# Performance work log

Measured on AMD Instinct MI355X. Metric: run time of the kernel, lower is better.

## Reference

```python
import jax, jax.numpy as jnp
import numpy as np

B, D_MODEL, N, H = 2, 1024, 2048, 16
HEAD_DIM = D_MODEL // H  # 64


def _proj(x, W, b):
    # Conv1d kernel_size=1 == per-position GEMM over channels. x: [B, Cin, N]
    return jnp.einsum('oi,bin->bon', W, x) + b[:, None]


def setup_inputs() -> dict:
    key = jax.random.key(0)
    ks = jax.random.split(key, 11)
    s = 1.0 / np.sqrt(D_MODEL)
    mk = lambda k: (jax.random.uniform(k, (D_MODEL, D_MODEL), jnp.float32, -s, s))
    return {
        'query': jax.random.normal(ks[0], (B, D_MODEL, N), jnp.float32),
        'key': jax.random.normal(ks[1], (B, D_MODEL, N), jnp.float32),
        'value': jax.random.normal(ks[2], (B, D_MODEL, N), jnp.float32),
        'Wq': mk(ks[3]), 'bq': jax.random.uniform(ks[4], (D_MODEL,), jnp.float32, -s, s),
        'Wk': mk(ks[5]), 'bk': jax.random.uniform(ks[6], (D_MODEL,), jnp.float32, -s, s),
        'Wv': mk(ks[7]), 'bv': jax.random.uniform(ks[8], (D_MODEL,), jnp.float32, -s, s),
        'Wm': mk(ks[9]), 'bm': jax.random.uniform(ks[10], (D_MODEL,), jnp.float32, -s, s),
    }


def reference(query, key, value, Wq, bq, Wk, bk, Wv, bv, Wm, bm):
    b = query.shape[0]
    # project then split channels as (head_dim, heads) exactly like torch .view
    q = _proj(query, Wq, bq).reshape(b, HEAD_DIM, H, -1)  # [B, d, H, N]
    k = _proj(key, Wk, bk).reshape(b, HEAD_DIM, H, -1)
    v = _proj(value, Wv, bv).reshape(b, HEAD_DIM, H, -1)
    scores = jnp.einsum('bdhn,bdhm->bhnm', q, k) / np.sqrt(HEAD_DIM).astype(np.float32)
    prob = jax.nn.softmax(scores, axis=-1)  # [B, H, N, N]
    x = jnp.einsum('bhnm,bdhm->bdhn', prob, v)  # [B, d, H, N]
    return _proj(x.reshape(b, D_MODEL, -1), Wm, bm)  # [B, d_model, N]
```

## Files before the change

kernel.cpp:

```cpp
#include <hip/hip_runtime.h>
#include <stdint.h>

#define DM 1024
#define NS 2048
#define NH 16
#define HD 64
#define SQ 72

typedef unsigned short u16;
typedef __attribute__((ext_vector_type(8))) short short8;
typedef __attribute__((ext_vector_type(8))) unsigned short u16x8;
typedef __attribute__((ext_vector_type(4))) float f32x4;
typedef __attribute__((ext_vector_type(4))) unsigned short u16x4;

static __device__ __forceinline__ u16 f2bf(float f) {
  union { float f; uint32_t i; } x; x.f = f;
  return (u16)((x.i + 0x7fffu + ((x.i >> 16) & 1u)) >> 16);
}
static __device__ __forceinline__ void gload16(u16* lds, const u16* g) {
  auto l = (__attribute__((address_space(3))) uint32_t*)(uint32_t)(uintptr_t)lds;
  auto gp = (const __attribute__((address_space(1))) uint32_t*)(uintptr_t)g;
  __builtin_amdgcn_global_load_lds(gp, l, 16, 0, 0);
}

__global__ __launch_bounds__(256) void cvt4_k(const float* __restrict__ a,
                                              const float* __restrict__ b,
                                              const float* __restrict__ c,
                                              const float* __restrict__ d,
                                              u16* __restrict__ oa, u16* __restrict__ ob,
                                              u16* __restrict__ oc, u16* __restrict__ od) {
  const int y = blockIdx.y;
  const float* in = y == 0 ? a : y == 1 ? b : y == 2 ? c : d;
  u16* out = y == 0 ? oa : y == 1 ? ob : y == 2 ? oc : od;
  int i = (blockIdx.x * 256 + threadIdx.x) * 4;
  f32x4 v = *(const f32x4*)(in + i);
  u16x4 o;
  o.x = f2bf(v.x); o.y = f2bf(v.y); o.z = f2bf(v.z); o.w = f2bf(v.w);
  *(u16x4*)(out + i) = o;
}

__global__ __launch_bounds__(256) void trf3_k(const float* __restrict__ q,
                                              const float* __restrict__ k,
                                              const float* __restrict__ v,
                                              u16* __restrict__ oq, u16* __restrict__ ok,
                                              u16* __restrict__ ov) {
  __shared__ __attribute__((aligned(16))) u16 t[64][65];
  const int z = blockIdx.z, b = z & 1, which = z >> 1;
  const float* in = which == 0 ? q : which == 1 ? k : v;
  u16* out = which == 0 ? oq : which == 1 ? ok : ov;
  const float* ip = in + (size_t)b * DM * NS;
  u16* op = out + (size_t)b * DM * NS;
  const int r0 = blockIdx.y * 64, c0 = blockIdx.x * 64;
  const int tx = threadIdx.x, ty = threadIdx.y;
#pragma unroll
  for (int j = 0; j < 4; ++j) {
    int row = ty + j * 16;
    f32x4 vv = *(const f32x4*)(ip + (size_t)(r0 + row) * NS + c0 + tx * 4);
    t[row][tx * 4 + 0] = f2bf(vv.x); t[row][tx * 4 + 1] = f2bf(vv.y);
    t[row][tx * 4 + 2] = f2bf(vv.z); t[row][tx * 4 + 3] = f2bf(vv.w);
  }
  __syncthreads();
#pragma unroll
  for (int j = 0; j < 4; ++j) {
    int crow = ty + j * 16;
    u16x4 vv;
    vv.x = t[tx * 4 + 0][crow]; vv.y = t[tx * 4 + 1][crow];
    vv.z = t[tx * 4 + 2][crow]; vv.w = t[tx * 4 + 3][crow];
    *(u16x4*)(op + (size_t)(c0 + crow) * DM + r0 + tx * 4) = vv;
  }
}

__global__ __launch_bounds__(256) void tr_k(const u16* __restrict__ in,
                                            u16* __restrict__ out) {
  __shared__ __attribute__((aligned(16))) u16 t[64][65];
  const int b = blockIdx.z;
  const u16* ip = in + (size_t)b * DM * NS;
  u16* op = out + (size_t)b * DM * NS;
  const int r0 = blockIdx.y * 64, c0 = blockIdx.x * 64;
  const int tx = threadIdx.x, ty = threadIdx.y;
#pragma unroll
  for (int j = 0; j < 4; ++j) {
    int row = ty + j * 16;
    u16x4 v = *(const u16x4*)(ip + (size_t)(r0 + row) * NS + c0 + tx * 4);
    t[row][tx * 4 + 0] = v.x; t[row][tx * 4 + 1] = v.y;
    t[row][tx * 4 + 2] = v.z; t[row][tx * 4 + 3] = v.w;
  }
  __syncthreads();
#pragma unroll
  for (int j = 0; j < 4; ++j) {
    int crow = ty + j * 16;
    u16x4 v;
    v.x = t[tx * 4 + 0][crow]; v.y = t[tx * 4 + 1][crow];
    v.z = t[tx * 4 + 2][crow]; v.w = t[tx * 4 + 3][crow];
    *(u16x4*)(op + (size_t)(c0 + crow) * DM + r0 + tx * 4) = v;
  }
}

__global__ __launch_bounds__(256) void qkv_k(
    const u16* __restrict__ Xq, const u16* __restrict__ Xk, const u16* __restrict__ Xv,
    const u16* __restrict__ Wq, const u16* __restrict__ Wk, const u16* __restrict__ Wv,
    const float* __restrict__ bq, const float* __restrict__ bk, const float* __restrict__ bv,
    u16* __restrict__ QH, u16* __restrict__ KH, u16* __restrict__ VH) {
  __shared__ __attribute__((aligned(16))) u16 As[128 * 32];
  __shared__ __attribute__((aligned(16))) u16 Bs[128 * 32];
  const int z = blockIdx.z, b = z & 1, which = z >> 1;
  const u16* X = which == 0 ? Xq : which == 1 ? Xk : Xv;
  const u16* W = which == 0 ? Wq : which == 1 ? Wk : Wv;
  const float* bias = which == 0 ? bq : which == 1 ? bk : bv;
  u16* out = which == 0 ? QH : which == 1 ? KH : VH;
  const int m0 = blockIdx.x * 128;
  const int c0 = blockIdx.y * 128;
  const u16* Xb = X + (size_t)b * NS * DM;
  const int tid = threadIdx.x;
  const int lane = tid & 63, w = tid >> 6;
  const int wm = w >> 1, wc = w & 1;
  const int qd = lane >> 4, ml = lane & 15;

  f32x4 acc[4][4];
#pragma unroll
  for (int i = 0; i < 4; ++i)
#pragma unroll
    for (int j = 0; j < 4; ++j) acc[i][j] = (f32x4){0.f, 0.f, 0.f, 0.f};

  for (int k0 = 0; k0 < DM; k0 += 32) {
    __syncthreads();
#pragma unroll
    for (int it = 0; it < 2; ++it) {
      int ci = it * 256 + tid;
      int row = ci >> 2, j = ci & 3;
      gload16(&As[ci * 8], Xb + (size_t)(m0 + row) * DM + k0 + j * 8);
      gload16(&Bs[ci * 8], W + (size_t)(c0 + row) * DM + k0 + j * 8);
    }
    __syncthreads();
    short8 af[4], bf[4];
#pragma unroll
    for (int i = 0; i < 4; ++i) {
      af[i] = *(const short8*)&As[(wm * 64 + i * 16 + ml) * 32 + qd * 8];
      bf[i] = *(const short8*)&Bs[(wc * 64 + i * 16 + ml) * 32 + qd * 8];
    }
#pragma unroll
    for (int mi = 0; mi < 4; ++mi)
#pragma unroll
      for (int ci2 = 0; ci2 < 4; ++ci2)
        acc[mi][ci2] = __builtin_amdgcn_mfma_f32_16x16x32_bf16(af[mi], bf[ci2],
                                                               acc[mi][ci2], 0, 0, 0);
  }

  const int cw = c0 + wc * 64;
  const int mw = m0 + wm * 64;
  float bv4[4];
#pragma unroll
  for (int ci2 = 0; ci2 < 4; ++ci2) bv4[ci2] = bias[cw + ci2 * 16 + ml];

  if (which < 2) {
    const int h = ml, d0 = cw >> 4;
    u16* ob = out + ((size_t)(b * NH + h) * NS) * HD;
#pragma unroll
    for (int mi = 0; mi < 4; ++mi) {
#pragma unroll
      for (int r = 0; r < 4; ++r) {
        int n = mw + mi * 16 + qd * 4 + r;
        u16x4 v;
        v.x = f2bf(acc[mi][0][r] + bv4[0]); v.y = f2bf(acc[mi][1][r] + bv4[1]);
        v.z = f2bf(acc[mi][2][r] + bv4[2]); v.w = f2bf(acc[mi][3][r] + bv4[3]);
        *(u16x4*)(ob + (size_t)n * HD + d0) = v;
      }
    }
  } else {
#pragma unroll
    for (int ci2 = 0; ci2 < 4; ++ci2) {
      int c = cw + ci2 * 16 + ml;
      int h = c & 15, d = c >> 4;
#pragma unroll
      for (int mi = 0; mi < 4; ++mi) {
        int nb = mw + mi * 16 + qd * 4;
        u16x4 v;
        v.x = f2bf(acc[mi][ci2][0] + bv4[ci2]); v.y = f2bf(acc[mi][ci2][1] + bv4[ci2]);
        v.z = f2bf(acc[mi][ci2][2] + bv4[ci2]); v.w = f2bf(acc[mi][ci2][3] + bv4[ci2]);
        *(u16x4*)(out + ((size_t)(b * NH + h) * HD + d) * NS + nb) = v;
      }
    }
  }
}

__global__ __launch_bounds__(256) void proj_o(const u16* __restrict__ X,
                                              const u16* __restrict__ W,
                                              const float* __restrict__ bias,
                                              float* __restrict__ out) {
  __shared__ __attribute__((aligned(16))) u16 As[128 * 32];
  __shared__ __attribute__((aligned(16))) u16 Bs[128 * 32];
  const int b = blockIdx.z;
  const int m0 = blockIdx.x * 128;
  const int c0 = blockIdx.y * 128;
  const u16* Xb = X + (size_t)b * NS * DM;
  const int tid = threadIdx.x;
  const int lane = tid & 63, w = tid >> 6;
  const int wm = w >> 1, wc = w & 1;
  const int qd = lane >> 4, ml = lane & 15;

  f32x4 acc[4][4];
#pragma unroll
  for (int i = 0; i < 4; ++i)
#pragma unroll
    for (int j = 0; j < 4; ++j) acc[i][j] = (f32x4){0.f, 0.f, 0.f, 0.f};

  for (int k0 = 0; k0 < DM; k0 += 32) {
    __syncthreads();
#pragma unroll
    for (int it = 0; it < 2; ++it) {
      int ci = it * 256 + tid;
      int row = ci >> 2, j = ci & 3;
      gload16(&As[ci * 8], Xb + (size_t)(m0 + row) * DM + k0 + j * 8);
      gload16(&Bs[ci * 8], W + (size_t)(c0 + row) * DM + k0 + j * 8);
    }
    __syncthreads();
    short8 af[4], bf[4];
#pragma unroll
    for (int i = 0; i < 4; ++i) {
      af[i] = *(const short8*)&As[(wm * 64 + i * 16 + ml) * 32 + qd * 8];
      bf[i] = *(const short8*)&Bs[(wc * 64 + i * 16 + ml) * 32 + qd * 8];
    }
#pragma unroll
    for (int mi = 0; mi < 4; ++mi)
#pragma unroll
      for (int ci2 = 0; ci2 < 4; ++ci2)
        acc[mi][ci2] = __builtin_amdgcn_mfma_f32_16x16x32_bf16(af[mi], bf[ci2],
                                                               acc[mi][ci2], 0, 0, 0);
  }

  const int cw = c0 + wc * 64;
  const int mw = m0 + wm * 64;
#pragma unroll
  for (int ci2 = 0; ci2 < 4; ++ci2) {
    int c = cw + ci2 * 16 + ml;
    float bv = bias[c];
#pragma unroll
    for (int mi = 0; mi < 4; ++mi) {
      int nb = mw + mi * 16 + qd * 4;
      f32x4 v;
      v.x = acc[mi][ci2][0] + bv; v.y = acc[mi][ci2][1] + bv;
      v.z = acc[mi][ci2][2] + bv; v.w = acc[mi][ci2][3] + bv;
      *(f32x4*)(out + ((size_t)b * DM + c) * NS + nb) = v;
    }
  }
}

__global__ __launch_bounds__(256) void attn_k(const u16* __restrict__ Q,
                                              const u16* __restrict__ K,
                                              const u16* __restrict__ V,
                                              u16* __restrict__ XO) {
  __shared__ __attribute__((aligned(16))) u16 QPs[64 * SQ];
  __shared__ __attribute__((aligned(16))) u16 Ks[64 * SQ];
  __shared__ __attribute__((aligned(16))) u16 Vs[64 * SQ];
  const int bh = blockIdx.y, b = bh >> 4, h = bh & 15;
  const int n0 = blockIdx.x * 64;
  const u16* Qb = Q + (size_t)bh * NS * HD;
  const u16* Kb = K + (size_t)bh * NS * HD;
  const u16* Vb = V + (size_t)bh * HD * NS;
  const int tid = threadIdx.x, lane = tid & 63, w = tid >> 6;
  const int qd = lane >> 4, ml = lane & 15;

#pragma unroll
  for (int it = 0; it < 2; ++it) {
    int ci = it * 256 + tid;
    int row = ci >> 3, j = ci & 7;
    *(u16x8*)&QPs[row * SQ + j * 8] = *(const u16x8*)(Qb + (size_t)(n0 + row) * HD + j * 8);
  }
  __syncthreads();
  short8 aq[2];
#pragma unroll
  for (int ks = 0; ks < 2; ++ks)
    aq[ks] = *(const short8*)&QPs[(w * 16 + ml) * SQ + (ks * 4 + qd) * 8];

  f32x4 O[4];
#pragma unroll
  for (int i = 0; i < 4; ++i) O[i] = (f32x4){0.f, 0.f, 0.f, 0.f};
  float lsum[4] = {0.f, 0.f, 0.f, 0.f};
  const float SC = 0.125f * 1.44269504088896340736f;

  const int srow = tid >> 3, sj = tid & 7;

  for (int kb = 0; kb < NS / 64; ++kb) {
    u16x8 kv[2], vv[2];
#pragma unroll
    for (int it = 0; it < 2; ++it) {
      kv[it] = *(const u16x8*)(Kb + (size_t)(kb * 64 + srow + it * 32) * HD + sj * 8);
      vv[it] = *(const u16x8*)(Vb + (size_t)(srow + it * 32) * NS + kb * 64 + sj * 8);
    }
    __syncthreads();
#pragma unroll
    for (int it = 0; it < 2; ++it) {
      *(u16x8*)&Ks[(srow + it * 32) * SQ + sj * 8] = kv[it];
      *(u16x8*)&Vs[(srow + it * 32) * SQ + sj * 8] = vv[it];
    }
    __syncthreads();

    f32x4 S[4];
#pragma unroll
    for (int f = 0; f < 4; ++f) S[f] = (f32x4){0.f, 0.f, 0.f, 0.f};
#pragma unroll
    for (int f = 0; f < 4; ++f)
#pragma unroll
      for (int ks = 0; ks < 2; ++ks) {
        short8 bk = *(const short8*)&Ks[(f * 16 + ml) * SQ + (ks * 4 + qd) * 8];
        S[f] = __builtin_amdgcn_mfma_f32_16x16x32_bf16(aq[ks], bk, S[f], 0, 0, 0);
      }

#pragma unroll
    for (int f = 0; f < 4; ++f)
#pragma unroll
      for (int r = 0; r < 4; ++r) {
        float p = __builtin_amdgcn_exp2f(S[f][r] * SC);
        QPs[(w * 16 + qd * 4 + r) * SQ + f * 16 + ml] = f2bf(p);
        lsum[r] += p;
      }
    __syncthreads();

#pragma unroll
    for (int kk = 0; kk < 2; ++kk) {
      short8 ap = *(const short8*)&QPs[(w * 16 + ml) * SQ + (kk * 4 + qd) * 8];
#pragma unroll
      for (int df = 0; df < 4; ++df) {
        short8 bvv = *(const short8*)&Vs[(df * 16 + ml) * SQ + (kk * 4 + qd) * 8];
        O[df] = __builtin_amdgcn_mfma_f32_16x16x32_bf16(ap, bvv, O[df], 0, 0, 0);
      }
    }
  }

#pragma unroll
  for (int off = 1; off < 16; off <<= 1)
#pragma unroll
    for (int r = 0; r < 4; ++r) lsum[r] += __shfl_xor(lsum[r], off);
#pragma unroll
  for (int r = 0; r < 4; ++r) lsum[r] = 1.f / lsum[r];

  const int nb = n0 + w * 16 + qd * 4;
#pragma unroll
  for (int df = 0; df < 4; ++df) {
    int d = df * 16 + ml;
    int c = d * NH + h;
    u16x4 v;
    v.x = f2bf(O[df][0] * lsum[0]); v.y = f2bf(O[df][1] * lsum[1]);
    v.z = f2bf(O[df][2] * lsum[2]); v.w = f2bf(O[df][3] * lsum[3]);
    *(u16x4*)(XO + ((size_t)b * DM + c) * NS + nb) = v;
  }
}

extern "C" void kernel_launch(void* const* d_in, const int* in_sizes, int n_in,
                              void* d_out, int out_size, void* d_ws, size_t ws_size,
                              hipStream_t stream) {
  const float* query = (const float*)d_in[0];
  const float* key = (const float*)d_in[1];
  const float* value = (const float*)d_in[2];
  const float* Wq = (const float*)d_in[3]; const float* bq = (const float*)d_in[4];
  const float* Wk = (const float*)d_in[5]; const float* bk = (const float*)d_in[6];
  const float* Wv = (const float*)d_in[7]; const float* bv = (const float*)d_in[8];
  const float* Wm = (const float*)d_in[9]; const float* bm = (const float*)d_in[10];

  u16* ws = (u16*)d_ws;
  const size_t TS = (size_t)2 * NS * DM;
  const size_t WSZ = (size_t)DM * DM;
  u16* XTq = ws;
  u16* XTk = ws + TS;
  u16* XTv = ws + 2 * TS;
  u16* QH = ws + 3 * TS;
  u16* KH = ws + 4 * TS;
  u16* VH = ws + 5 * TS;
  u16* Wqb = ws + 6 * TS;
  u16* Wkb = Wqb + WSZ;
  u16* Wvb = Wkb + WSZ;
  u16* Wmb = Wvb + WSZ;
  u16* XO = XTq;
  u16* XOT = XTk;

  cvt4_k<<<dim3(WSZ / 1024, 4), 256, 0, stream>>>(Wq, Wk, Wv, Wm, Wqb, Wkb, Wvb, Wmb);

  dim3 tb(16, 16);
  trf3_k<<<dim3(NS / 64, DM / 64, 6), tb, 0, stream>>>(query, key, value, XTq, XTk, XTv);

  qkv_k<<<dim3(NS / 128, DM / 128, 6), 256, 0, stream>>>(
      XTq, XTk, XTv, Wqb, Wkb, Wvb, bq, bk, bv, QH, KH, VH);

  attn_k<<<dim3(NS / 64, 32), 256, 0, stream>>>(QH, KH, VH, XO);

  tr_k<<<dim3(NS / 64, DM / 64, 2), tb, 0, stream>>>(XO, XOT);
  proj_o<<<dim3(NS / 128, DM / 128, 2), 256, 0, stream>>>(XOT, Wmb, bm, (float*)d_out);
}
```

Baseline: 262.9 us.

## Split attention over key halves with combine kernel, fold softmax scale into Q

```diff
diff --git a/kernel.cpp b/kernel.cpp
--- a/kernel.cpp
+++ b/kernel.cpp
@@ -108,6 +108,7 @@
   const u16* W = which == 0 ? Wq : which == 1 ? Wk : Wv;
   const float* bias = which == 0 ? bq : which == 1 ? bk : bv;
   u16* out = which == 0 ? QH : which == 1 ? KH : VH;
+  const float sc = which == 0 ? 0.18033688011112042f : 1.0f;
   const int m0 = blockIdx.x * 128;
   const int c0 = blockIdx.y * 128;
   const u16* Xb = X + (size_t)b * NS * DM;
@@ -161,8 +162,10 @@
       for (int r = 0; r < 4; ++r) {
         int n = mw + mi * 16 + qd * 4 + r;
         u16x4 v;
-        v.x = f2bf(acc[mi][0][r] + bv4[0]); v.y = f2bf(acc[mi][1][r] + bv4[1]);
-        v.z = f2bf(acc[mi][2][r] + bv4[2]); v.w = f2bf(acc[mi][3][r] + bv4[3]);
+        v.x = f2bf((acc[mi][0][r] + bv4[0]) * sc);
+        v.y = f2bf((acc[mi][1][r] + bv4[1]) * sc);
+        v.z = f2bf((acc[mi][2][r] + bv4[2]) * sc);
+        v.w = f2bf((acc[mi][3][r] + bv4[3]) * sc);
         *(u16x4*)(ob + (size_t)n * HD + d0) = v;
       }
     }
@@ -187,10 +190,10 @@
                                               const u16* __restrict__ W,
                                               const float* __restrict__ bias,
                                               float* __restrict__ out) {
-  __shared__ __attribute__((aligned(16))) u16 As[128 * 32];
+  __shared__ __attribute__((aligned(16))) u16 As[64 * 32];
   __shared__ __attribute__((aligned(16))) u16 Bs[128 * 32];
   const int b = blockIdx.z;
-  const int m0 = blockIdx.x * 128;
+  const int m0 = blockIdx.x * 64;
   const int c0 = blockIdx.y * 128;
   const u16* Xb = X + (size_t)b * NS * DM;
   const int tid = threadIdx.x;
@@ -198,30 +201,34 @@
   const int wm = w >> 1, wc = w & 1;
   const int qd = lane >> 4, ml = lane & 15;
 
-  f32x4 acc[4][4];
-#pragma unroll
-  for (int i = 0; i < 4; ++i)
+  f32x4 acc[2][4];
+#pragma unroll
+  for (int i = 0; i < 2; ++i)
 #pragma unroll
     for (int j = 0; j < 4; ++j) acc[i][j] = (f32x4){0.f, 0.f, 0.f, 0.f};
 
   for (int k0 = 0; k0 < DM; k0 += 32) {
     __syncthreads();
+    {
+      int row = tid >> 2, j = tid & 3;
+      gload16(&As[tid * 8], Xb + (size_t)(m0 + row) * DM + k0 + j * 8);
+    }
 #pragma unroll
     for (int it = 0; it < 2; ++it) {
       int ci = it * 256 + tid;
       int row = ci >> 2, j = ci & 3;
-      gload16(&As[ci * 8], Xb + (size_t)(m0 + row) * DM + k0 + j * 8);
       gload16(&Bs[ci * 8], W + (size_t)(c0 + row) * DM + k0 + j * 8);
     }
     __syncthreads();
-    short8 af[4], bf[4];
-#pragma unroll
-    for (int i = 0; i < 4; ++i) {
-      af[i] = *(const short8*)&As[(wm * 64 + i * 16 + ml) * 32 + qd * 8];
+    short8 af[2], bf[4];
+#pragma unroll
+    for (int i = 0; i < 2; ++i)
+      af[i] = *(const short8*)&As[(wm * 32 + i * 16 + ml) * 32 + qd * 8];
+#pragma unroll
+    for (int i = 0; i < 4; ++i)
       bf[i] = *(const short8*)&Bs[(wc * 64 + i * 16 + ml) * 32 + qd * 8];
-    }
-#pragma unroll
-    for (int mi = 0; mi < 4; ++mi)
+#pragma unroll
+    for (int mi = 0; mi < 2; ++mi)
 #pragma unroll
       for (int ci2 = 0; ci2 < 4; ++ci2)
         acc[mi][ci2] = __builtin_amdgcn_mfma_f32_16x16x32_bf16(af[mi], bf[ci2],
@@ -229,13 +236,13 @@
   }
 
   const int cw = c0 + wc * 64;
-  const int mw = m0 + wm * 64;
+  const int mw = m0 + wm * 32;
 #pragma unroll
   for (int ci2 = 0; ci2 < 4; ++ci2) {
     int c = cw + ci2 * 16 + ml;
     float bv = bias[c];
 #pragma unroll
-    for (int mi = 0; mi < 4; ++mi) {
+    for (int mi = 0; mi < 2; ++mi) {
       int nb = mw + mi * 16 + qd * 4;
       f32x4 v;
       v.x = acc[mi][ci2][0] + bv; v.y = acc[mi][ci2][1] + bv;
@@ -248,15 +255,18 @@
 __global__ __launch_bounds__(256) void attn_k(const u16* __restrict__ Q,
                                               const u16* __restrict__ K,
                                               const u16* __restrict__ V,
-                                              u16* __restrict__ XO) {
+                                              float* __restrict__ O0,
+                                              float* __restrict__ O1,
+                                              float* __restrict__ lp) {
   __shared__ __attribute__((aligned(16))) u16 QPs[64 * SQ];
   __shared__ __attribute__((aligned(16))) u16 Ks[64 * SQ];
   __shared__ __attribute__((aligned(16))) u16 Vs[64 * SQ];
   const int bh = blockIdx.y, b = bh >> 4, h = bh & 15;
+  const int half = blockIdx.z;
   const int n0 = blockIdx.x * 64;
   const u16* Qb = Q + (size_t)bh * NS * HD;
-  const u16* Kb = K + (size_t)bh * NS * HD;
-  const u16* Vb = V + (size_t)bh * HD * NS;
+  const u16* Kb = K + (size_t)bh * NS * HD + (size_t)half * (NS / 2) * HD;
+  const u16* Vb = V + (size_t)bh * HD * NS + (size_t)half * (NS / 2);
   const int tid = threadIdx.x, lane = tid & 63, w = tid >> 6;
   const int qd = lane >> 4, ml = lane & 15;
 
@@ -276,11 +286,10 @@
 #pragma unroll
   for (int i = 0; i < 4; ++i) O[i] = (f32x4){0.f, 0.f, 0.f, 0.f};
   float lsum[4] = {0.f, 0.f, 0.f, 0.f};
-  const float SC = 0.125f * 1.44269504088896340736f;
 
   const int srow = tid >> 3, sj = tid & 7;
 
-  for (int kb = 0; kb < NS / 64; ++kb) {
+  for (int kb = 0; kb < (NS / 2) / 64; ++kb) {
     u16x8 kv[2], vv[2];
 #pragma unroll
     for (int it = 0; it < 2; ++it) {
@@ -310,7 +319,7 @@
     for (int f = 0; f < 4; ++f)
 #pragma unroll
       for (int r = 0; r < 4; ++r) {
-        float p = __builtin_amdgcn_exp2f(S[f][r] * SC);
+        float p = __builtin_amdgcn_exp2f(S[f][r]);
         QPs[(w * 16 + qd * 4 + r) * SQ + f * 16 + ml] = f2bf(p);
         lsum[r] += p;
       }
@@ -331,19 +340,40 @@
   for (int off = 1; off < 16; off <<= 1)
 #pragma unroll
     for (int r = 0; r < 4; ++r) lsum[r] += __shfl_xor(lsum[r], off);
-#pragma unroll
-  for (int r = 0; r < 4; ++r) lsum[r] = 1.f / lsum[r];
-
+
+  float* Op = half ? O1 : O0;
   const int nb = n0 + w * 16 + qd * 4;
+  if (ml == 0) {
+    f32x4 lv = {lsum[0], lsum[1], lsum[2], lsum[3]};
+    *(f32x4*)(lp + ((size_t)(half * 32 + bh)) * NS + nb) = lv;
+  }
 #pragma unroll
   for (int df = 0; df < 4; ++df) {
     int d = df * 16 + ml;
     int c = d * NH + h;
-    u16x4 v;
-    v.x = f2bf(O[df][0] * lsum[0]); v.y = f2bf(O[df][1] * lsum[1]);
-    v.z = f2bf(O[df][2] * lsum[2]); v.w = f2bf(O[df][3] * lsum[3]);
-    *(u16x4*)(XO + ((size_t)b * DM + c) * NS + nb) = v;
-  }
+    *(f32x4*)(Op + ((size_t)b * DM + c) * NS + nb) = O[df];
+  }
+}
+
+__global__ __launch_bounds__(256) void comb_k(const float* __restrict__ O0,
+                                              const float* __restrict__ O1,
+                                              const float* __restrict__ lp,
+                                              u16* __restrict__ XO) {
+  const size_t t = (size_t)blockIdx.x * 256 + threadIdx.x;
+  const int n4 = (int)(t & (NS / 4 - 1));
+  const int c = (int)((t >> 9) & (DM - 1));
+  const int b = (int)(t >> 19);
+  const int h = c & 15;
+  f32x4 o0 = *(const f32x4*)(O0 + t * 4);
+  f32x4 o1 = *(const f32x4*)(O1 + t * 4);
+  f32x4 l0 = *(const f32x4*)(lp + ((size_t)(b * 16 + h)) * NS + n4 * 4);
+  f32x4 l1 = *(const f32x4*)(lp + ((size_t)(32 + b * 16 + h)) * NS + n4 * 4);
+  u16x4 v;
+  v.x = f2bf((o0.x + o1.x) / (l0.x + l1.x));
+  v.y = f2bf((o0.y + o1.y) / (l0.y + l1.y));
+  v.z = f2bf((o0.z + o1.z) / (l0.z + l1.z));
+  v.w = f2bf((o0.w + o1.w) / (l0.w + l1.w));
+  *(u16x4*)(XO + t * 4) = v;
 }
 
 extern "C" void kernel_launch(void* const* d_in, const int* in_sizes, int n_in,
@@ -370,8 +400,11 @@
   u16* Wkb = Wqb + WSZ;
   u16* Wvb = Wkb + WSZ;
   u16* Wmb = Wvb + WSZ;
-  u16* XO = XTq;
-  u16* XOT = XTk;
+  float* O0 = (float*)ws;
+  float* O1 = (float*)(ws + 6 * TS + 4 * WSZ);
+  float* lp = O1 + (size_t)2 * DM * NS;
+  u16* XO = XTv;
+  u16* XOT = QH;
 
   cvt4_k<<<dim3(WSZ / 1024, 4), 256, 0, stream>>>(Wq, Wk, Wv, Wm, Wqb, Wkb, Wvb, Wmb);
 
@@ -381,8 +414,10 @@
   qkv_k<<<dim3(NS / 128, DM / 128, 6), 256, 0, stream>>>(
       XTq, XTk, XTv, Wqb, Wkb, Wvb, bq, bk, bv, QH, KH, VH);
 
-  attn_k<<<dim3(NS / 64, 32), 256, 0, stream>>>(QH, KH, VH, XO);
+  attn_k<<<dim3(NS / 64, 32, 2), 256, 0, stream>>>(QH, KH, VH, O0, O1, lp);
+
+  comb_k<<<dim3((DM * NS * 2 / 4) / 256), 256, 0, stream>>>(O0, O1, lp, XO);
 
   tr_k<<<dim3(NS / 64, DM / 64, 2), tb, 0, stream>>>(XO, XOT);
-  proj_o<<<dim3(NS / 128, DM / 128, 2), 256, 0, stream>>>(XOT, Wmb, bm, (float*)d_out);
-}
+  proj_o<<<dim3(NS / 64, DM / 128, 2), 256, 0, stream>>>(XOT, Wmb, bm, (float*)d_out);
+}
```

Result: no change. 266.8 us (+1.5%).

## Restructure attention with double-buffered async K/V loads and register-resident P

Applied to the files above, without the earlier changes.

```diff
diff --git a/kernel.cpp b/kernel.cpp
--- a/kernel.cpp
+++ b/kernel.cpp
@@ -5,13 +5,15 @@
 #define NS 2048
 #define NH 16
 #define HD 64
-#define SQ 72
 
 typedef unsigned short u16;
 typedef __attribute__((ext_vector_type(8))) short short8;
+typedef __attribute__((ext_vector_type(4))) short s16x4;
 typedef __attribute__((ext_vector_type(8))) unsigned short u16x8;
 typedef __attribute__((ext_vector_type(4))) float f32x4;
 typedef __attribute__((ext_vector_type(4))) unsigned short u16x4;
+
+#define MFMA_PV(a, b, c) __builtin_amdgcn_mfma_f32_16x16x16bf16_1k(a, b, c, 0, 0, 0)
 
 static __device__ __forceinline__ u16 f2bf(float f) {
   union { float f; uint32_t i; } x; x.f = f;
@@ -108,6 +110,7 @@
   const u16* W = which == 0 ? Wq : which == 1 ? Wk : Wv;
   const float* bias = which == 0 ? bq : which == 1 ? bk : bv;
   u16* out = which == 0 ? QH : which == 1 ? KH : VH;
+  const float sc = which == 0 ? 0.18033688011112042f : 1.0f;
   const int m0 = blockIdx.x * 128;
   const int c0 = blockIdx.y * 128;
   const u16* Xb = X + (size_t)b * NS * DM;
@@ -161,8 +164,10 @@
       for (int r = 0; r < 4; ++r) {
         int n = mw + mi * 16 + qd * 4 + r;
         u16x4 v;
-        v.x = f2bf(acc[mi][0][r] + bv4[0]); v.y = f2bf(acc[mi][1][r] + bv4[1]);
-        v.z = f2bf(acc[mi][2][r] + bv4[2]); v.w = f2bf(acc[mi][3][r] + bv4[3]);
+        v.x = f2bf((acc[mi][0][r] + bv4[0]) * sc);
+        v.y = f2bf((acc[mi][1][r] + bv4[1]) * sc);
+        v.z = f2bf((acc[mi][2][r] + bv4[2]) * sc);
+        v.w = f2bf((acc[mi][3][r] + bv4[3]) * sc);
         *(u16x4*)(ob + (size_t)n * HD + d0) = v;
       }
     }
@@ -187,10 +192,10 @@
                                               const u16* __restrict__ W,
                                               const float* __restrict__ bias,
                                               float* __restrict__ out) {
-  __shared__ __attribute__((aligned(16))) u16 As[128 * 32];
+  __shared__ __attribute__((aligned(16))) u16 As[64 * 32];
   __shared__ __attribute__((aligned(16))) u16 Bs[128 * 32];
   const int b = blockIdx.z;
-  const int m0 = blockIdx.x * 128;
+  const int m0 = blockIdx.x * 64;
   const int c0 = blockIdx.y * 128;
   const u16* Xb = X + (size_t)b * NS * DM;
   const int tid = threadIdx.x;
@@ -198,30 +203,34 @@
   const int wm = w >> 1, wc = w & 1;
   const int qd = lane >> 4, ml = lane & 15;
 
-  f32x4 acc[4][4];
-#pragma unroll
-  for (int i = 0; i < 4; ++i)
+  f32x4 acc[2][4];
+#pragma unroll
+  for (int i = 0; i < 2; ++i)
 #pragma unroll
     for (int j = 0; j < 4; ++j) acc[i][j] = (f32x4){0.f, 0.f, 0.f, 0.f};
 
   for (int k0 = 0; k0 < DM; k0 += 32) {
     __syncthreads();
+    {
+      int row = tid >> 2, j = tid & 3;
+      gload16(&As[tid * 8], Xb + (size_t)(m0 + row) * DM + k0 + j * 8);
+    }
 #pragma unroll
     for (int it = 0; it < 2; ++it) {
       int ci = it * 256 + tid;
       int row = ci >> 2, j = ci & 3;
-      gload16(&As[ci * 8], Xb + (size_t)(m0 + row) * DM + k0 + j * 8);
       gload16(&Bs[ci * 8], W + (size_t)(c0 + row) * DM + k0 + j * 8);
     }
     __syncthreads();
-    short8 af[4], bf[4];
-#pragma unroll
-    for (int i = 0; i < 4; ++i) {
-      af[i] = *(const short8*)&As[(wm * 64 + i * 16 + ml) * 32 + qd * 8];
+    short8 af[2], bf[4];
+#pragma unroll
+    for (int i = 0; i < 2; ++i)
+      af[i] = *(const short8*)&As[(wm * 32 + i * 16 + ml) * 32 + qd * 8];
+#pragma unroll
+    for (int i = 0; i < 4; ++i)
       bf[i] = *(const short8*)&Bs[(wc * 64 + i * 16 + ml) * 32 + qd * 8];
-    }
-#pragma unroll
-    for (int mi = 0; mi < 4; ++mi)
+#pragma unroll
+    for (int mi = 0; mi < 2; ++mi)
 #pragma unroll
       for (int ci2 = 0; ci2 < 4; ++ci2)
         acc[mi][ci2] = __builtin_amdgcn_mfma_f32_16x16x32_bf16(af[mi], bf[ci2],
@@ -229,13 +238,13 @@
   }
 
   const int cw = c0 + wc * 64;
-  const int mw = m0 + wm * 64;
+  const int mw = m0 + wm * 32;
 #pragma unroll
   for (int ci2 = 0; ci2 < 4; ++ci2) {
     int c = cw + ci2 * 16 + ml;
     float bv = bias[c];
 #pragma unroll
-    for (int mi = 0; mi < 4; ++mi) {
+    for (int mi = 0; mi < 2; ++mi) {
       int nb = mw + mi * 16 + qd * 4;
       f32x4 v;
       v.x = acc[mi][ci2][0] + bv; v.y = acc[mi][ci2][1] + bv;
@@ -249,9 +258,8 @@
                                               const u16* __restrict__ K,
                                               const u16* __restrict__ V,
                                               u16* __restrict__ XO) {
-  __shared__ __attribute__((aligned(16))) u16 QPs[64 * SQ];
-  __shared__ __attribute__((aligned(16))) u16 Ks[64 * SQ];
-  __shared__ __attribute__((aligned(16))) u16 Vs[64 * SQ];
+  __shared__ __attribute__((aligned(16))) u16 Ks[2 * 2 * 2048];
+  __shared__ __attribute__((aligned(16))) u16 Vs[2 * 2 * 2048];
   const int bh = blockIdx.y, b = bh >> 4, h = bh & 15;
   const int n0 = blockIdx.x * 64;
   const u16* Qb = Q + (size_t)bh * NS * HD;
@@ -260,79 +268,86 @@
   const int tid = threadIdx.x, lane = tid & 63, w = tid >> 6;
   const int qd = lane >> 4, ml = lane & 15;
 
-#pragma unroll
-  for (int it = 0; it < 2; ++it) {
-    int ci = it * 256 + tid;
-    int row = ci >> 3, j = ci & 7;
-    *(u16x8*)&QPs[row * SQ + j * 8] = *(const u16x8*)(Qb + (size_t)(n0 + row) * HD + j * 8);
+  short8 aq[2];
+  {
+    const u16* qr = Qb + (size_t)(n0 + w * 16 + ml) * HD + qd * 8;
+    aq[0] = *(const short8*)qr;
+    aq[1] = *(const short8*)(qr + 32);
+  }
+
+  const int srow = tid >> 2, sjj = tid & 3;
+  const int vjj = sjj ^ (srow & 3);
+
+#pragma unroll
+  for (int s = 0; s < 2; ++s) {
+    gload16(&Ks[s * 2048 + tid * 8], Kb + (size_t)srow * HD + s * 32 + sjj * 8);
+    gload16(&Vs[s * 2048 + tid * 8], Vb + (size_t)srow * NS + s * 32 + vjj * 8);
   }
   __syncthreads();
-  short8 aq[2];
-#pragma unroll
-  for (int ks = 0; ks < 2; ++ks)
-    aq[ks] = *(const short8*)&QPs[(w * 16 + ml) * SQ + (ks * 4 + qd) * 8];
 
   f32x4 O[4];
 #pragma unroll
   for (int i = 0; i < 4; ++i) O[i] = (f32x4){0.f, 0.f, 0.f, 0.f};
-  float lsum[4] = {0.f, 0.f, 0.f, 0.f};
-  const float SC = 0.125f * 1.44269504088896340736f;
-
-  const int srow = tid >> 3, sj = tid & 7;
+  float lsum = 0.f;
+
+  const int vperm[2] = {(qd >> 1) ^ (ml & 3), (2 + (qd >> 1)) ^ (ml & 3)};
+  const int vhalf = (qd & 1) * 4;
 
   for (int kb = 0; kb < NS / 64; ++kb) {
-    u16x8 kv[2], vv[2];
-#pragma unroll
-    for (int it = 0; it < 2; ++it) {
-      kv[it] = *(const u16x8*)(Kb + (size_t)(kb * 64 + srow + it * 32) * HD + sj * 8);
-      vv[it] = *(const u16x8*)(Vb + (size_t)(srow + it * 32) * NS + kb * 64 + sj * 8);
+    const int cur = kb & 1, nxt = cur ^ 1;
+    if (kb < NS / 64 - 1) {
+#pragma unroll
+      for (int s = 0; s < 2; ++s) {
+        gload16(&Ks[(nxt * 2 + s) * 2048 + tid * 8],
+                Kb + (size_t)((kb + 1) * 64 + srow) * HD + s * 32 + sjj * 8);
+        gload16(&Vs[(nxt * 2 + s) * 2048 + tid * 8],
+                Vb + (size_t)srow * NS + (kb + 1) * 64 + s * 32 + vjj * 8);
+      }
+    }
+
+    const u16* kbase = &Ks[cur * 2 * 2048];
+    f32x4 S[4];
+#pragma unroll
+    for (int f = 0; f < 4; ++f) S[f] = (f32x4){0.f, 0.f, 0.f, 0.f};
+#pragma unroll
+    for (int f = 0; f < 4; ++f)
+#pragma unroll
+      for (int ks = 0; ks < 2; ++ks) {
+        short8 bk = *(const short8*)&kbase[ks * 2048 + (f * 16 + ml) * 32 + qd * 8];
+        S[f] = __builtin_amdgcn_mfma_f32_16x16x32_bf16(bk, aq[ks], S[f], 0, 0, 0);
+      }
+
+    s16x4 pf[4];
+#pragma unroll
+    for (int f = 0; f < 4; ++f) {
+      float p0 = __builtin_amdgcn_exp2f(S[f][0]);
+      float p1 = __builtin_amdgcn_exp2f(S[f][1]);
+      float p2 = __builtin_amdgcn_exp2f(S[f][2]);
+      float p3 = __builtin_amdgcn_exp2f(S[f][3]);
+      lsum += (p0 + p1) + (p2 + p3);
+      pf[f] = (s16x4){(short)f2bf(p0), (short)f2bf(p1),
+                      (short)f2bf(p2), (short)f2bf(p3)};
+    }
+
+    const u16* vbase = &Vs[cur * 2 * 2048];
+#pragma unroll
+    for (int t = 0; t < 4; ++t) {
+      const int vs = t >> 1;
+      const int voff = vperm[t & 1] * 8 + vhalf;
+#pragma unroll
+      for (int df = 0; df < 4; ++df) {
+        s16x4 vb = *(const s16x4*)&vbase[vs * 2048 + (df * 16 + ml) * 32 + voff];
+        O[df] = MFMA_PV(pf[t], vb, O[df]);
+      }
     }
     __syncthreads();
-#pragma unroll
-    for (int it = 0; it < 2; ++it) {
-      *(u16x8*)&Ks[(srow + it * 32) * SQ + sj * 8] = kv[it];
-      *(u16x8*)&Vs[(srow + it * 32) * SQ + sj * 8] = vv[it];
-    }
-    __syncthreads();
-
-    f32x4 S[4];
-#pragma unroll
-    for (int f = 0; f < 4; ++f) S[f] = (f32x4){0.f, 0.f, 0.f, 0.f};
-#pragma unroll
-    for (int f = 0; f < 4; ++f)
-#pragma unroll
-      for (int ks = 0; ks < 2; ++ks) {
-        short8 bk = *(const short8*)&Ks[(f * 16 + ml) * SQ + (ks * 4 + qd) * 8];
-        S[f] = __builtin_amdgcn_mfma_f32_16x16x32_bf16(aq[ks], bk, S[f], 0, 0, 0);
-      }
-
-#pragma unroll
-    for (int f = 0; f < 4; ++f)
-#pragma unroll
-      for (int r = 0; r < 4; ++r) {
-        float p = __builtin_amdgcn_exp2f(S[f][r] * SC);
-        QPs[(w * 16 + qd * 4 + r) * SQ + f * 16 + ml] = f2bf(p);
-        lsum[r] += p;
-      }
-    __syncthreads();
-
-#pragma unroll
-    for (int kk = 0; kk < 2; ++kk) {
-      short8 ap = *(const short8*)&QPs[(w * 16 + ml) * SQ + (kk * 4 + qd) * 8];
-#pragma unroll
-      for (int df = 0; df < 4; ++df) {
-        short8 bvv = *(const short8*)&Vs[(df * 16 + ml) * SQ + (kk * 4 + qd) * 8];
-        O[df] = __builtin_amdgcn_mfma_f32_16x16x32_bf16(ap, bvv, O[df], 0, 0, 0);
-      }
-    }
-  }
-
-#pragma unroll
-  for (int off = 1; off < 16; off <<= 1)
-#pragma unroll
-    for (int r = 0; r < 4; ++r) lsum[r] += __shfl_xor(lsum[r], off);
-#pragma unroll
-  for (int r = 0; r < 4; ++r) lsum[r] = 1.f / lsum[r];
+  }
+
+  lsum += __shfl_xor(lsum, 16);
+  lsum += __shfl_xor(lsum, 32);
+  float linv[4];
+#pragma unroll
+  for (int r = 0; r < 4; ++r) linv[r] = 1.f / __shfl(lsum, qd * 4 + r);
 
   const int nb = n0 + w * 16 + qd * 4;
 #pragma unroll
@@ -340,8 +355,8 @@
     int d = df * 16 + ml;
     int c = d * NH + h;
     u16x4 v;
-    v.x = f2bf(O[df][0] * lsum[0]); v.y = f2bf(O[df][1] * lsum[1]);
-    v.z = f2bf(O[df][2] * lsum[2]); v.w = f2bf(O[df][3] * lsum[3]);
+    v.x = f2bf(O[df][0] * linv[0]); v.y = f2bf(O[df][1] * linv[1]);
+    v.z = f2bf(O[df][2] * linv[2]); v.w = f2bf(O[df][3] * linv[3]);
     *(u16x4*)(XO + ((size_t)b * DM + c) * NS + nb) = v;
   }
 }
@@ -384,5 +399,5 @@
   attn_k<<<dim3(NS / 64, 32), 256, 0, stream>>>(QH, KH, VH, XO);
 
   tr_k<<<dim3(NS / 64, DM / 64, 2), tb, 0, stream>>>(XO, XOT);
-  proj_o<<<dim3(NS / 128, DM / 128, 2), 256, 0, stream>>>(XOT, Wmb, bm, (float*)d_out);
-}
+  proj_o<<<dim3(NS / 64, DM / 128, 2), 256, 0, stream>>>(XOT, Wmb, bm, (float*)d_out);
+}
```

Result: no change. 263.5 us (+0.2%).
